# Kernel optimization log

Hardware: AMD Instinct MI355X
Metric: run time of the kernel (lower is better)

Reference implementation:

```python
import jax, jax.numpy as jnp
import numpy as np

N = 1_000_000
D = 128
B = 1024  # number of graphs in the batch


def setup_inputs() -> dict:
    key = jax.random.key(0)
    k1, k2, k3 = jax.random.split(key, 3)
    feat = jax.random.normal(k1, (N, D), dtype=jnp.float32)
    w_gate = jax.random.normal(k2, (D, 1), dtype=jnp.float32) * 0.02
    b_gate = jnp.zeros((1,), dtype=jnp.float32)
    segment_ids = jnp.sort(jax.random.randint(k3, (N,), 0, B, dtype=jnp.int32))
    return {"feat": feat, "w_gate": w_gate, "b_gate": b_gate,
            "segment_ids": segment_ids}


def reference(feat, w_gate, b_gate, segment_ids):
    # gate_nn: Linear(D, 1) -> per-node scalar score
    gate = (feat @ w_gate + b_gate)[:, 0]                      # [N]
    # softmax_nodes: per-graph (segment) numerically stable softmax
    seg_max = jax.ops.segment_max(gate, segment_ids, num_segments=B)   # [B]
    e = jnp.exp(gate - seg_max[segment_ids])                   # [N]
    seg_sum = jax.ops.segment_sum(e, segment_ids, num_segments=B)      # [B]
    alpha = e / seg_sum[segment_ids]                           # [N]
    # sum_nodes of feat * gate: weighted per-graph readout
    readout = jax.ops.segment_sum(feat * alpha[:, None], segment_ids,
                                  num_segments=B)              # [B, D]
    return readout, alpha[:, None]
```

## Files before the change

kernel.cpp:

```cpp
#include <hip/hip_runtime.h>
#include <math.h>

__global__ __launch_bounds__(256) void k_segstart(
        const int* __restrict__ seg, int* __restrict__ segstart, int N, int B) {
    int i = blockIdx.x * blockDim.x + threadIdx.x;
    if (i >= N) return;
    int s = seg[i];
    int p = (i == 0) ? -1 : seg[i - 1];
    for (int bb = p + 1; bb <= s; ++bb) segstart[bb] = i;
    if (i == N - 1)
        for (int bb = s + 1; bb <= B; ++bb) segstart[bb] = N;
}

template <int CTRL>
__device__ __forceinline__ float dpp_add(float v) {
    int sh = __builtin_amdgcn_update_dpp(0, __float_as_int(v), CTRL, 0xF, 0xF,
                                         false);
    return v + __int_as_float(sh);
}
__device__ __forceinline__ float halfwave_sum(float v) {
    v = dpp_add<0xB1>(v);
    v = dpp_add<0x4E>(v);
    v = dpp_add<0x141>(v);
    v = dpp_add<0x140>(v);
    int sw = __builtin_amdgcn_ds_swizzle(__float_as_int(v), 0x401F);
    return v + __int_as_float(sw);
}

__global__ __launch_bounds__(256, 4) void k_pool(
        const float* __restrict__ feat, const float* __restrict__ w,
        const float* __restrict__ bptr, const int* __restrict__ segstart,
        float* __restrict__ gbuf, float* __restrict__ Mbuf,
        float* __restrict__ invbuf, float* __restrict__ readout) {
    int b = blockIdx.x;
    int start = segstart[b], end = segstart[b + 1];
    int t = threadIdx.x, rg = t >> 5, cl = t & 31;

    const float4 w4 = ((const float4*)w)[cl];
    const float bias = bptr[0];
    const float4* featv = (const float4*)feat;

    float m = -INFINITY, s = 0.0f;
    float4 acc = make_float4(0.0f, 0.0f, 0.0f, 0.0f);

    const int len = end - start;
    const int nfull = len >> 6;
    const float4* rowp = featv + (size_t)(start + rg) * 32 + cl;
    const bool cl0 = (cl == 0);

    float4 f[8], p[8];

#define PROCESS8(rowbase)                                                     \
    do {                                                                      \
        float g[8];                                                           \
        _Pragma("unroll") for (int j = 0; j < 8; ++j)                         \
            g[j] = f[j].x * w4.x + f[j].y * w4.y + f[j].z * w4.z +            \
                   f[j].w * w4.w;                                             \
        _Pragma("unroll") for (int j = 0; j < 8; ++j)                         \
            g[j] = dpp_add<0xB1>(g[j]);                                       \
        _Pragma("unroll") for (int j = 0; j < 8; ++j)                         \
            g[j] = dpp_add<0x4E>(g[j]);                                       \
        _Pragma("unroll") for (int j = 0; j < 8; ++j)                         \
            g[j] = dpp_add<0x141>(g[j]);                                      \
        _Pragma("unroll") for (int j = 0; j < 8; ++j)                         \
            g[j] = dpp_add<0x140>(g[j]);                                      \
        _Pragma("unroll") for (int j = 0; j < 8; ++j) {                       \
            int sw = __builtin_amdgcn_ds_swizzle(__float_as_int(g[j]),        \
                                                 0x401F);                     \
            g[j] = g[j] + __int_as_float(sw) + bias;                          \
        }                                                                     \
        if (cl0) {                                                            \
            _Pragma("unroll") for (int j = 0; j < 8; ++j)                     \
                gbuf[(rowbase) + 8 * j] = g[j];                               \
        }                                                                     \
        float gm = fmaxf(fmaxf(fmaxf(g[0], g[1]), fmaxf(g[2], g[3])),         \
                         fmaxf(fmaxf(g[4], g[5]), fmaxf(g[6], g[7])));        \
        if (gm > m) {                                                         \
            float r = __expf(m - gm);         \
            s *= r;                                                           \
            acc.x *= r; acc.y *= r; acc.z *= r; acc.w *= r;                   \
            m = gm;                                                           \
        }                                                                     \
        float e[8];                                                           \
        _Pragma("unroll") for (int j = 0; j < 8; ++j)                         \
            e[j] = __expf(g[j] - m);                                          \
        s += ((e[0] + e[1]) + (e[2] + e[3])) +                                \
             ((e[4] + e[5]) + (e[6] + e[7]));                                 \
        _Pragma("unroll") for (int j = 0; j < 8; ++j) {                       \
            acc.x += f[j].x * e[j]; acc.y += f[j].y * e[j];                   \
            acc.z += f[j].z * e[j]; acc.w += f[j].w * e[j];                   \
        }                                                                     \
    } while (0)

    if (nfull > 0) {
        #pragma unroll
        for (int j = 0; j < 8; ++j) f[j] = rowp[(size_t)j * 256];
        for (int it = 1; it < nfull; ++it) {
            const float4* nxt = rowp + (size_t)it * 2048;
            #pragma unroll
            for (int j = 0; j < 8; ++j) p[j] = nxt[(size_t)j * 256];
            PROCESS8(start + rg + (it - 1) * 64);
            #pragma unroll
            for (int j = 0; j < 8; ++j) f[j] = p[j];
        }
        PROCESS8(start + rg + (nfull - 1) * 64);
    }

    for (int n = start + nfull * 64 + rg; n < end; n += 8) {
        float4 ft = featv[(size_t)n * 32 + cl];
        float g = halfwave_sum(ft.x * w4.x + ft.y * w4.y + ft.z * w4.z +
                               ft.w * w4.w) + bias;
        if (cl0) gbuf[n] = g;
        if (g > m) {
            float r = __expf(m - g);
            s *= r;
            acc.x *= r; acc.y *= r; acc.z *= r; acc.w *= r;
            m = g;
        }
        float e = __expf(g - m);
        s += e;
        acc.x += ft.x * e; acc.y += ft.y * e; acc.z += ft.z * e;
        acc.w += ft.w * e;
    }

    __shared__ float mred[8], sred[8];
    if (cl0) { mred[rg] = m; sred[rg] = s; }
    __syncthreads();
    float M = -INFINITY;
    #pragma unroll
    for (int g2 = 0; g2 < 8; ++g2) M = fmaxf(M, mred[g2]);
    float S = 0.0f;
    #pragma unroll
    for (int g2 = 0; g2 < 8; ++g2)
        if (sred[g2] > 0.0f) S += sred[g2] * __expf(mred[g2] - M);
    const float inv = (S > 0.0f) ? 1.0f / S : 0.0f;

    float r = (s > 0.0f) ? __expf(m - M) : 0.0f;
    acc.x *= r; acc.y *= r; acc.z *= r; acc.w *= r;

    __shared__ float4 red[256];
    red[t] = acc;
    __syncthreads();
    #pragma unroll
    for (int off = 4; off >= 1; off >>= 1) {
        if (rg < off) {
            float4 o = red[t + off * 32];
            red[t].x += o.x; red[t].y += o.y; red[t].z += o.z; red[t].w += o.w;
        }
        __syncthreads();
    }
    if (rg == 0) {
        float4 o = red[t];
        o.x *= inv; o.y *= inv; o.z *= inv; o.w *= inv;
        ((float4*)(readout + (size_t)b * 128))[cl] = o;
    }
    if (t == 0) { Mbuf[b] = M; invbuf[b] = inv; }
}

__global__ __launch_bounds__(256) void k_alpha(
        const float* __restrict__ gbuf, const int* __restrict__ seg,
        const float* __restrict__ Mbuf, const float* __restrict__ invbuf,
        float* __restrict__ alpha, int N) {
    int i = blockIdx.x * blockDim.x + threadIdx.x;
    int i4 = i * 4;
    if (i4 + 3 < N) {
        float4 g = ((const float4*)gbuf)[i];
        int4 sv = ((const int4*)seg)[i];
        float4 a;
        a.x = __expf(g.x - Mbuf[sv.x]) * invbuf[sv.x];
        a.y = __expf(g.y - Mbuf[sv.y]) * invbuf[sv.y];
        a.z = __expf(g.z - Mbuf[sv.z]) * invbuf[sv.z];
        a.w = __expf(g.w - Mbuf[sv.w]) * invbuf[sv.w];
        ((float4*)alpha)[i] = a;
    } else if (i4 < N) {
        for (int k = i4; k < N; ++k) {
            int sb = seg[k];
            alpha[k] = __expf(gbuf[k] - Mbuf[sb]) * invbuf[sb];
        }
    }
}

extern "C" void kernel_launch(void* const* d_in, const int* in_sizes, int n_in,
                              void* d_out, int out_size, void* d_ws, size_t ws_size,
                              hipStream_t stream) {
    const float* feat  = (const float*)d_in[0];
    const float* wgate = (const float*)d_in[1];
    const float* bgate = (const float*)d_in[2];
    const int*   seg   = (const int*)d_in[3];

    const int N = in_sizes[3];
    const int D = in_sizes[1];
    const int B = (out_size - N) / D;

    float* readout = (float*)d_out;
    float* alpha   = (float*)d_out + (size_t)B * 128;

    int* segstart = (int*)d_ws;
    size_t off = (((size_t)(B + 1) * 4) + 255) & ~(size_t)255;
    float* Mbuf = (float*)((char*)d_ws + off);
    float* invbuf = Mbuf + B;
    size_t off2 = (off + (size_t)2 * B * 4 + 255) & ~(size_t)255;
    float* gbuf = (float*)((char*)d_ws + off2);

    k_segstart<<<(N + 255) / 256, 256, 0, stream>>>(seg, segstart, N, B);
    k_pool<<<B, 256, 0, stream>>>(feat, wgate, bgate, segstart,
                                  gbuf, Mbuf, invbuf, readout);
    int threads4 = (N + 3) / 4;
    k_alpha<<<(threads4 + 255) / 256, 256, 0, stream>>>(gbuf, seg, Mbuf, invbuf,
                                                        alpha, N);
}
```

Before: 665.6 us.

## Split each segment across two blocks and merge partial softmax in combine kernel

The pooling kernel now launches two blocks per graph, each handling half of the segment's rows and writing partial max, sum and weighted accumulators to workspace. A new small combine kernel merges the two partials with rescaling and writes the readout plus the per-graph max and inverse sum. The inner loop is cut from 8 rows to 4 rows per step and the launch-bounds occupancy hint is dropped. This aims to use more of the GPU's compute units, since 1024 blocks is few for the device, and to lower register pressure. In exchange it adds an extra kernel launch and a partial-buffer round trip, and each block has less prefetch depth.

```diff
diff --git a/kernel.cpp b/kernel.cpp
--- a/kernel.cpp
+++ b/kernel.cpp
@@ -1,5 +1,7 @@
 #include <hip/hip_runtime.h>
 #include <math.h>
+
+typedef float f4 __attribute__((ext_vector_type(4)));
 
 __global__ __launch_bounds__(256) void k_segstart(
         const int* __restrict__ seg, int* __restrict__ segstart, int N, int B) {
@@ -27,100 +29,102 @@
     return v + __int_as_float(sw);
 }
 
-__global__ __launch_bounds__(256, 4) void k_pool(
+__global__ __launch_bounds__(256) void k_pool_partial(
         const float* __restrict__ feat, const float* __restrict__ w,
         const float* __restrict__ bptr, const int* __restrict__ segstart,
-        float* __restrict__ gbuf, float* __restrict__ Mbuf,
-        float* __restrict__ invbuf, float* __restrict__ readout) {
-    int b = blockIdx.x;
-    int start = segstart[b], end = segstart[b + 1];
-    int t = threadIdx.x, rg = t >> 5, cl = t & 31;
-
-    const float4 w4 = ((const float4*)w)[cl];
+        float* __restrict__ gbuf, float* __restrict__ pm,
+        float* __restrict__ ps, f4* __restrict__ pacc) {
+    const int bp = blockIdx.x;
+    const int b = bp >> 1, half = bp & 1;
+    const int start = segstart[b], end = segstart[b + 1];
+    const int len = end - start;
+    const int hlen = (len + 1) >> 1;
+    const int s0 = start + half * hlen;
+    const int e0 = (s0 + hlen < end) ? (s0 + hlen) : end;
+
+    const int t = threadIdx.x, rg = t >> 5, cl = t & 31;
+    const bool cl0 = (cl == 0);
+
+    const f4 w4 = ((const f4*)w)[cl];
     const float bias = bptr[0];
-    const float4* featv = (const float4*)feat;
+    const f4* featv = (const f4*)feat;
 
     float m = -INFINITY, s = 0.0f;
-    float4 acc = make_float4(0.0f, 0.0f, 0.0f, 0.0f);
-
-    const int len = end - start;
-    const int nfull = len >> 6;
-    const float4* rowp = featv + (size_t)(start + rg) * 32 + cl;
-    const bool cl0 = (cl == 0);
-
-    float4 f[8], p[8];
-
-#define PROCESS8(rowbase)                                                     \
+    f4 acc = (f4)0.0f;
+
+    const int plen = (e0 > s0) ? (e0 - s0) : 0;
+    const int nfull = plen >> 5;
+    const f4* rowp = featv + ((size_t)s0 + rg) * 32 + cl;
+
+    f4 f0, f1, f2, f3;
+
+#define PROCESS4(rowbase)                                                     \
     do {                                                                      \
-        float g[8];                                                           \
-        _Pragma("unroll") for (int j = 0; j < 8; ++j)                         \
-            g[j] = f[j].x * w4.x + f[j].y * w4.y + f[j].z * w4.z +            \
-                   f[j].w * w4.w;                                             \
-        _Pragma("unroll") for (int j = 0; j < 8; ++j)                         \
-            g[j] = dpp_add<0xB1>(g[j]);                                       \
-        _Pragma("unroll") for (int j = 0; j < 8; ++j)                         \
-            g[j] = dpp_add<0x4E>(g[j]);                                       \
-        _Pragma("unroll") for (int j = 0; j < 8; ++j)                         \
-            g[j] = dpp_add<0x141>(g[j]);                                      \
-        _Pragma("unroll") for (int j = 0; j < 8; ++j)                         \
-            g[j] = dpp_add<0x140>(g[j]);                                      \
-        _Pragma("unroll") for (int j = 0; j < 8; ++j) {                       \
-            int sw = __builtin_amdgcn_ds_swizzle(__float_as_int(g[j]),        \
-                                                 0x401F);                     \
-            g[j] = g[j] + __int_as_float(sw) + bias;                          \
+        float g0 = f0.x * w4.x + f0.y * w4.y + f0.z * w4.z + f0.w * w4.w;     \
+        float g1 = f1.x * w4.x + f1.y * w4.y + f1.z * w4.z + f1.w * w4.w;     \
+        float g2 = f2.x * w4.x + f2.y * w4.y + f2.z * w4.z + f2.w * w4.w;     \
+        float g3 = f3.x * w4.x + f3.y * w4.y + f3.z * w4.z + f3.w * w4.w;     \
+        g0 = dpp_add<0xB1>(g0); g1 = dpp_add<0xB1>(g1);                       \
+        g2 = dpp_add<0xB1>(g2); g3 = dpp_add<0xB1>(g3);                       \
+        g0 = dpp_add<0x4E>(g0); g1 = dpp_add<0x4E>(g1);                       \
+        g2 = dpp_add<0x4E>(g2); g3 = dpp_add<0x4E>(g3);                       \
+        g0 = dpp_add<0x141>(g0); g1 = dpp_add<0x141>(g1);                     \
+        g2 = dpp_add<0x141>(g2); g3 = dpp_add<0x141>(g3);                     \
+        g0 = dpp_add<0x140>(g0); g1 = dpp_add<0x140>(g1);                     \
+        g2 = dpp_add<0x140>(g2); g3 = dpp_add<0x140>(g3);                     \
+        g0 += __int_as_float(__builtin_amdgcn_ds_swizzle(                     \
+                 __float_as_int(g0), 0x401F)) + bias;                         \
+        g1 += __int_as_float(__builtin_amdgcn_ds_swizzle(                     \
+                 __float_as_int(g1), 0x401F)) + bias;                         \
+        g2 += __int_as_float(__builtin_amdgcn_ds_swizzle(                     \
+                 __float_as_int(g2), 0x401F)) + bias;                         \
+        g3 += __int_as_float(__builtin_amdgcn_ds_swizzle(                     \
+                 __float_as_int(g3), 0x401F)) + bias;                         \
+        if (cl0) {                                                            \
+            gbuf[(rowbase)] = g0;                                             \
+            gbuf[(rowbase) + 8] = g1;                                         \
+            gbuf[(rowbase) + 16] = g2;                                        \
+            gbuf[(rowbase) + 24] = g3;                                        \
         }                                                                     \
-        if (cl0) {                                                            \
-            _Pragma("unroll") for (int j = 0; j < 8; ++j)                     \
-                gbuf[(rowbase) + 8 * j] = g[j];                               \
-        }                                                                     \
-        float gm = fmaxf(fmaxf(fmaxf(g[0], g[1]), fmaxf(g[2], g[3])),         \
-                         fmaxf(fmaxf(g[4], g[5]), fmaxf(g[6], g[7])));        \
+        float gm = fmaxf(fmaxf(g0, g1), fmaxf(g2, g3));                       \
         if (gm > m) {                                                         \
             float r = __expf(m - gm);         \
-            s *= r;                                                           \
-            acc.x *= r; acc.y *= r; acc.z *= r; acc.w *= r;                   \
-            m = gm;                                                           \
+            s *= r; acc *= r; m = gm;                                         \
         }                                                                     \
-        float e[8];                                                           \
-        _Pragma("unroll") for (int j = 0; j < 8; ++j)                         \
-            e[j] = __expf(g[j] - m);                                          \
-        s += ((e[0] + e[1]) + (e[2] + e[3])) +                                \
-             ((e[4] + e[5]) + (e[6] + e[7]));                                 \
-        _Pragma("unroll") for (int j = 0; j < 8; ++j) {                       \
-            acc.x += f[j].x * e[j]; acc.y += f[j].y * e[j];                   \
-            acc.z += f[j].z * e[j]; acc.w += f[j].w * e[j];                   \
-        }                                                                     \
+        float e0_ = __expf(g0 - m), e1_ = __expf(g1 - m);                     \
+        float e2_ = __expf(g2 - m), e3_ = __expf(g3 - m);                     \
+        s += (e0_ + e1_) + (e2_ + e3_);                                       \
+        acc += f0 * e0_; acc += f1 * e1_;                                     \
+        acc += f2 * e2_; acc += f3 * e3_;                                     \
     } while (0)
 
     if (nfull > 0) {
-        #pragma unroll
-        for (int j = 0; j < 8; ++j) f[j] = rowp[(size_t)j * 256];
+        f0 = rowp[0];
+        f1 = rowp[256];
+        f2 = rowp[512];
+        f3 = rowp[768];
+        #pragma unroll 2
         for (int it = 1; it < nfull; ++it) {
-            const float4* nxt = rowp + (size_t)it * 2048;
-            #pragma unroll
-            for (int j = 0; j < 8; ++j) p[j] = nxt[(size_t)j * 256];
-            PROCESS8(start + rg + (it - 1) * 64);
-            #pragma unroll
-            for (int j = 0; j < 8; ++j) f[j] = p[j];
+            const f4* nx = rowp + (size_t)it * 1024;
+            f4 p0 = nx[0], p1 = nx[256], p2 = nx[512], p3 = nx[768];
+            PROCESS4(s0 + rg + (it - 1) * 32);
+            f0 = p0; f1 = p1; f2 = p2; f3 = p3;
         }
-        PROCESS8(start + rg + (nfull - 1) * 64);
-    }
-
-    for (int n = start + nfull * 64 + rg; n < end; n += 8) {
-        float4 ft = featv[(size_t)n * 32 + cl];
+        PROCESS4(s0 + rg + (nfull - 1) * 32);
+    }
+
+    for (int n = s0 + nfull * 32 + rg; n < e0; n += 8) {
+        f4 ft = featv[(size_t)n * 32 + cl];
         float g = halfwave_sum(ft.x * w4.x + ft.y * w4.y + ft.z * w4.z +
                                ft.w * w4.w) + bias;
         if (cl0) gbuf[n] = g;
         if (g > m) {
             float r = __expf(m - g);
-            s *= r;
-            acc.x *= r; acc.y *= r; acc.z *= r; acc.w *= r;
-            m = g;
+            s *= r; acc *= r; m = g;
         }
         float e = __expf(g - m);
         s += e;
-        acc.x += ft.x * e; acc.y += ft.y * e; acc.z += ft.z * e;
-        acc.w += ft.w * e;
+        acc += ft * e;
     }
 
     __shared__ float mred[8], sred[8];
@@ -133,28 +137,42 @@
     #pragma unroll
     for (int g2 = 0; g2 < 8; ++g2)
         if (sred[g2] > 0.0f) S += sred[g2] * __expf(mred[g2] - M);
-    const float inv = (S > 0.0f) ? 1.0f / S : 0.0f;
 
     float r = (s > 0.0f) ? __expf(m - M) : 0.0f;
-    acc.x *= r; acc.y *= r; acc.z *= r; acc.w *= r;
-
-    __shared__ float4 red[256];
+    acc *= r;
+
+    __shared__ f4 red[256];
     red[t] = acc;
     __syncthreads();
     #pragma unroll
     for (int off = 4; off >= 1; off >>= 1) {
-        if (rg < off) {
-            float4 o = red[t + off * 32];
-            red[t].x += o.x; red[t].y += o.y; red[t].z += o.z; red[t].w += o.w;
-        }
+        if (rg < off) red[t] += red[t + off * 32];
         __syncthreads();
     }
-    if (rg == 0) {
-        float4 o = red[t];
-        o.x *= inv; o.y *= inv; o.z *= inv; o.w *= inv;
-        ((float4*)(readout + (size_t)b * 128))[cl] = o;
-    }
+    if (rg == 0) pacc[(size_t)bp * 32 + cl] = red[t];
+    if (t == 0) { pm[bp] = M; ps[bp] = S; }
+}
+
+__global__ __launch_bounds__(64) void k_combine(
+        const float* __restrict__ pm, const float* __restrict__ ps,
+        const f4* __restrict__ pacc, float* __restrict__ Mbuf,
+        float* __restrict__ invbuf, float* __restrict__ readout) {
+    const int b = blockIdx.x, t = threadIdx.x;
+    const float M0 = pm[2 * b], M1 = pm[2 * b + 1];
+    const float S0 = ps[2 * b], S1 = ps[2 * b + 1];
+    const float M = fmaxf(M0, M1);
+    const float c0 = (S0 > 0.0f) ? __expf(M0 - M) : 0.0f;
+    const float c1 = (S1 > 0.0f) ? __expf(M1 - M) : 0.0f;
+    const float S = S0 * c0 + S1 * c1;
+    const float inv = (S > 0.0f) ? 1.0f / S : 0.0f;
     if (t == 0) { Mbuf[b] = M; invbuf[b] = inv; }
+    if (t < 32) {
+        f4 a0 = pacc[(size_t)(2 * b) * 32 + t];
+        f4 a1 = pacc[(size_t)(2 * b + 1) * 32 + t];
+        f4 rr = a0 * c0 + a1 * c1;
+        rr *= inv;
+        ((f4*)readout)[(size_t)b * 32 + t] = rr;
+    }
 }
 
 __global__ __launch_bounds__(256) void k_alpha(
@@ -164,14 +182,14 @@
     int i = blockIdx.x * blockDim.x + threadIdx.x;
     int i4 = i * 4;
     if (i4 + 3 < N) {
-        float4 g = ((const float4*)gbuf)[i];
+        f4 g = ((const f4*)gbuf)[i];
         int4 sv = ((const int4*)seg)[i];
-        float4 a;
+        f4 a;
         a.x = __expf(g.x - Mbuf[sv.x]) * invbuf[sv.x];
         a.y = __expf(g.y - Mbuf[sv.y]) * invbuf[sv.y];
         a.z = __expf(g.z - Mbuf[sv.z]) * invbuf[sv.z];
         a.w = __expf(g.w - Mbuf[sv.w]) * invbuf[sv.w];
-        ((float4*)alpha)[i] = a;
+        ((f4*)alpha)[i] = a;
     } else if (i4 < N) {
         for (int k = i4; k < N; ++k) {
             int sb = seg[k];
@@ -195,16 +213,23 @@
     float* readout = (float*)d_out;
     float* alpha   = (float*)d_out + (size_t)B * 128;
 
-    int* segstart = (int*)d_ws;
+    char* ws = (char*)d_ws;
+    int* segstart = (int*)ws;
     size_t off = (((size_t)(B + 1) * 4) + 255) & ~(size_t)255;
-    float* Mbuf = (float*)((char*)d_ws + off);
+    float* Mbuf = (float*)(ws + off);
     float* invbuf = Mbuf + B;
-    size_t off2 = (off + (size_t)2 * B * 4 + 255) & ~(size_t)255;
-    float* gbuf = (float*)((char*)d_ws + off2);
+    off = (off + (size_t)2 * B * 4 + 255) & ~(size_t)255;
+    float* pm = (float*)(ws + off);
+    float* ps = pm + 2 * B;
+    off = (off + (size_t)4 * B * 4 + 255) & ~(size_t)255;
+    f4* pacc = (f4*)(ws + off);
+    off = (off + (size_t)2 * B * 128 * 4 + 255) & ~(size_t)255;
+    float* gbuf = (float*)(ws + off);
 
     k_segstart<<<(N + 255) / 256, 256, 0, stream>>>(seg, segstart, N, B);
-    k_pool<<<B, 256, 0, stream>>>(feat, wgate, bgate, segstart,
-                                  gbuf, Mbuf, invbuf, readout);
+    k_pool_partial<<<2 * B, 256, 0, stream>>>(feat, wgate, bgate, segstart,
+                                              gbuf, pm, ps, pacc);
+    k_combine<<<B, 64, 0, stream>>>(pm, ps, pacc, Mbuf, invbuf, readout);
     int threads4 = (N + 3) / 4;
     k_alpha<<<(threads4 + 255) / 256, 256, 0, stream>>>(gbuf, seg, Mbuf, invbuf,
                                                         alpha, N);
```

Measured after the change: 667.3 us. No clear change (+0.3%).
